# Kernel tuning notes

Hardware: AMD Instinct MI355X
Metric: run time of the kernel (lower is better)

Reference implementation:

```python
import jax, jax.numpy as jnp
import numpy as np

BLOCK_LEN = 64

def _segsum(x):
    # x: (..., T) -> (..., T, T) with entry [t, s] = sum_{u=s+1..t} x[u], -inf above diagonal
    T = x.shape[-1]
    cs = jnp.cumsum(x, axis=-1)
    ss = cs[..., :, None] - cs[..., None, :]
    mask = jnp.tril(jnp.ones((T, T), dtype=bool))
    return jnp.where(mask, ss, -jnp.inf)

def setup_inputs() -> dict:
    key = jax.random.key(0)
    kx, ka, kb, kc = jax.random.split(key, 4)
    b, L, h, p, n = 4, 4096, 32, 64, 16
    X = jax.random.normal(kx, (b, L, h, p), dtype=jnp.float32)
    # negative, small-magnitude A so exp(cumsum(A)) stays finite (decaying SSM),
    # matching the math of the module while keeping the baseline numerically sane
    A = -0.1 * jnp.abs(jax.random.normal(ka, (b, L, h), dtype=jnp.float32))
    B = jax.random.normal(kb, (b, L, h, n), dtype=jnp.float32)
    C = jax.random.normal(kc, (b, L, h, n), dtype=jnp.float32)
    return {"X": X, "A": A, "B": B, "C": C}

def reference(X, A, B, C):
    b, L, h, p = X.shape
    n = B.shape[-1]
    l = BLOCK_LEN
    c = L // l
    # chunk into blocks
    Xb = X.reshape(b, c, l, h, p)                       # b c l h p
    Ab = A.reshape(b, c, l, h).transpose(0, 3, 1, 2)    # b h c l
    Bb = B.reshape(b, c, l, h, n)                       # b c l h n
    Cb = C.reshape(b, c, l, h, n)                       # b c l h n
    A_cumsum = jnp.cumsum(Ab, axis=-1)                  # b h c l
    # intra-chunk (diagonal) term; equals the fused per-timestep scan
    # h_t = exp(A_t)*h_{t-1} + B_t*x_t ; y_t = C_t . h_t
    Lmat = jnp.exp(_segsum(Ab))                         # b h c l l (lower-tri)
    Y_diag = jnp.einsum('bclhn,bcshn,bhcls,bcshp->bclhp', Cb, Bb, Lmat, Xb)
    # per-chunk end states
    decay_states = jnp.exp(A_cumsum[..., -1:] - A_cumsum)  # b h c l
    states = jnp.einsum('bclhn,bhcl,bclhp->bchpn', Bb, decay_states, Xb)
    states = jnp.concatenate([jnp.zeros_like(states[:, :1]), states], axis=1)  # b (c+1) h p n
    # inter-chunk recurrence via segment-sum of chunk totals
    decay_chunk = jnp.exp(_segsum(jnp.pad(A_cumsum[..., -1], ((0, 0), (0, 0), (1, 0)))))  # b h (c+1) (c+1)
    new_states = jnp.einsum('bhzc,bchpn->bzhpn', decay_chunk, states)
    states = new_states[:, :-1]                          # b c h p n
    # state -> output contribution
    state_decay_out = jnp.exp(A_cumsum)                  # b h c l
    Y_off = jnp.einsum('bclhn,bchpn,bhcl->bclhp', Cb, states, state_decay_out)
    return (Y_diag + Y_off).reshape(b, L, h, p)
```

## Files before the change

### kernel.cpp

```cpp
#include <hip/hip_runtime.h>

#define BATCH   4
#define SEQLEN  4096
#define NHEADS  32
#define PDIM    64
#define NDIM    16
#define CHUNK   64
#define NCHUNK  64
#define PHALF   32

typedef short v8s __attribute__((ext_vector_type(8)));
typedef float v4f __attribute__((ext_vector_type(4)));

union V8U { v8s s; unsigned u[4]; };

__device__ __forceinline__ short f2bf(float f) {
    union { float f; unsigned u; } x; x.f = f;
    unsigned r = (x.u + 0x7FFFu + ((x.u >> 16) & 1u)) >> 16;
    return (short)r;
}
__device__ __forceinline__ float bf2f(short s) {
    union { unsigned u; float f; } x; x.u = ((unsigned)(unsigned short)s) << 16;
    return x.f;
}
__device__ __forceinline__ unsigned cvt_pk_bf16(float lo, float hi) {
    unsigned r;
    asm("v_cvt_pk_bf16_f32 %0, %1, %2" : "=v"(r) : "v"(lo), "v"(hi));
    return r;
}

__device__ __forceinline__ float wave_iscan(float v, int lane) {
#pragma unroll
    for (int d = 1; d < 64; d <<= 1) {
        float o = __shfl_up(v, (unsigned)d, 64);
        if (lane >= d) v += o;
    }
    return v;
}

__global__ __launch_bounds__(512) void k_fused(
    const float* __restrict__ X, const float* __restrict__ A,
    const float* __restrict__ Bm, const float* __restrict__ Cm,
    float* __restrict__ Y)
{
    const int ph = blockIdx.x, hh = blockIdx.y, bb = blockIdx.z;
    const int tid = threadIdx.x;
    const int lane = tid & 63;
    const int wv = tid >> 6;
    const int W = wv & 3;
    const int qq = lane >> 4, nn = lane & 15;

    __shared__ __align__(16) float sCumAll[SEQLEN];
    __shared__ __align__(16) short xF [4][4][64][8];
    __shared__ __align__(16) short xSF[4][4][64][8];
    __shared__ __align__(16) short cFq[4][2048];
    __shared__ __align__(16) short bFq[4][2048];
    __shared__ __align__(16) short bFs[4][1024];
    __shared__ __align__(16) short sF [4][1024];
    __shared__ __align__(16) float gRaw[CHUNK][68];
    __shared__ float wtot[8];

    {
        const v8s z8 = {0,0,0,0,0,0,0,0};
        ((v8s*)cFq)[tid] = z8; ((v8s*)cFq)[tid + 512] = z8;
        ((v8s*)bFq)[tid] = z8; ((v8s*)bFq)[tid + 512] = z8;
        if (tid < 128) ((v8s*)sF)[tid] = z8;
    }

    {
        const float* Ab = A + (size_t)bb * SEQLEN * NHEADS + hh;
        const int tb = wv * 512 + lane * 8;
        float av[8];
#pragma unroll
        for (int j = 0; j < 8; ++j) av[j] = Ab[(size_t)(tb + j) * NHEADS];
        float s8 = 0.f;
#pragma unroll
        for (int j = 0; j < 8; ++j) s8 += av[j];
        const float pre = wave_iscan(s8, lane);
        if (lane == 63) wtot[wv] = pre;
        __syncthreads();
        float base = 0.f;
#pragma unroll
        for (int w = 0; w < 7; ++w) if (w < wv) base += wtot[w];
        float c = base + pre - s8;
#pragma unroll
        for (int j = 0; j < 8; ++j) { c += av[j]; sCumAll[tb + j] = c; }
        __syncthreads();
    }

    auto stage = [&](int c, int buf) {
        const int t0c = bb * SEQLEN + c * CHUNK;
        const float* gcc = &sCumAll[c * CHUNK];
        const int ti = wv - 4, kk = ti >> 1, nt = ti & 1;
        const int trow = kk * 32 + qq * 8;
        const float* xb = X + ((size_t)(t0c + trow) * NHEADS + hh) * PDIM
                            + ph * PHALF + nt * 16 + nn;
        float xv[8];
#pragma unroll
        for (int j = 0; j < 8; ++j) xv[j] = xb[(size_t)j * (NHEADS * PDIM)];
        const float gtot = gcc[63];
        float ex[8];
#pragma unroll
        for (int j = 0; j < 8; ++j) ex[j] = __expf(gtot - gcc[trow + j]);
        V8U xf, xs;
#pragma unroll
        for (int j2 = 0; j2 < 4; ++j2) {
            xf.u[j2] = cvt_pk_bf16(xv[2*j2], xv[2*j2+1]);
            xs.u[j2] = cvt_pk_bf16(xv[2*j2] * ex[2*j2], xv[2*j2+1] * ex[2*j2+1]);
        }
        *(v8s*)&xF [buf][kk*2+nt][lane][0] = xf.s;
        *(v8s*)&xSF[buf][kk*2+nt][lane][0] = xs.s;
        const int ptid = tid & 255;
        const int r = ptid >> 2, n0 = (ptid & 3) * 4;
        const float4 bv = *(const float4*)&Bm[((size_t)(t0c + r) * NHEADS + hh) * NDIM + n0];
        const int offq = ((r >> 4) * 64 + (n0 >> 3) * 16 + (r & 15)) * 8 + (n0 & 7);
        bFq[buf][offq + 0] = f2bf(bv.x); bFq[buf][offq + 1] = f2bf(bv.y);
        bFq[buf][offq + 2] = f2bf(bv.z); bFq[buf][offq + 3] = f2bf(bv.w);
        const int kb = r >> 5, qb = (r >> 3) & 3, jj = r & 7;
        const int bs = (kb * 64 + qb * 16) * 8 + jj;
        bFs[buf][bs + (n0 + 0) * 8] = f2bf(bv.x);
        bFs[buf][bs + (n0 + 1) * 8] = f2bf(bv.y);
        bFs[buf][bs + (n0 + 2) * 8] = f2bf(bv.z);
        bFs[buf][bs + (n0 + 3) * 8] = f2bf(bv.w);
        const float4 cv = *(const float4*)&Cm[((size_t)(t0c + r) * NHEADS + hh) * NDIM + n0];
        cFq[buf][offq + 0] = f2bf(cv.x); cFq[buf][offq + 1] = f2bf(cv.y);
        cFq[buf][offq + 2] = f2bf(cv.z); cFq[buf][offq + 3] = f2bf(cv.w);
    };

    const v4f zero = {0.f, 0.f, 0.f, 0.f};

    auto qk_g = [&](const float* gc, int buf) -> v8s {
        const v8s cfrag = *(const v8s*)&cFq[buf][(W * 64 + lane) * 8];
        float tc[4];
#pragma unroll
        for (int r = 0; r < 4; ++r) tc[r] = gc[W * 16 + qq * 4 + r];
#pragma unroll
        for (int st = 0; st < 4; ++st) {
            if (st <= W) {
                const v8s bfrag = *(const v8s*)&bFq[buf][(st * 64 + lane) * 8];
                v4f acc = __builtin_amdgcn_mfma_f32_16x16x32_bf16(cfrag, bfrag, zero, 0, 0, 0);
                const float cums = gc[st * 16 + nn];
#pragma unroll
                for (int r = 0; r < 4; ++r) {
                    const int t = W * 16 + qq * 4 + r;
                    const int s = st * 16 + nn;
                    gRaw[t][s] = (t >= s) ? acc[r] * __expf(tc[r] - cums) : 0.f;
                }
            }
        }
        if (W == 0) {
#pragma unroll
            for (int r = 0; r < 4; ++r) gRaw[qq * 4 + r][16 + nn] = 0.f;
        } else if (W == 2) {
#pragma unroll
            for (int r = 0; r < 4; ++r) gRaw[32 + qq * 4 + r][48 + nn] = 0.f;
        }
        return cfrag;
    };

    auto do_y = [&](const float* gc, float gbase, int buf, int t0c, v8s cfrag) {
        const float et = __expf(gc[W * 16 + nn] - gbase);
        V8U cef;
#pragma unroll
        for (int j2 = 0; j2 < 4; ++j2)
            cef.u[j2] = cvt_pk_bf16(bf2f(cfrag[2*j2]) * et, bf2f(cfrag[2*j2+1]) * et);
        V8U ga0u, ga1u;
        {
            const float* gr = &gRaw[W * 16 + nn][qq * 8];
#pragma unroll
            for (int j2 = 0; j2 < 4; ++j2) ga0u.u[j2] = cvt_pk_bf16(gr[2*j2], gr[2*j2+1]);
        }
        const bool usekk1 = (W >= 2);
        if (usekk1) {
            const float* gr = &gRaw[W * 16 + nn][32 + qq * 8];
#pragma unroll
            for (int j2 = 0; j2 < 4; ++j2) ga1u.u[j2] = cvt_pk_bf16(gr[2*j2], gr[2*j2+1]);
        }
        v4f ya[2];
#pragma unroll
        for (int nt2 = 0; nt2 < 2; ++nt2) {
            const v8s sfrag = *(const v8s*)&sF[buf][(nt2 * 64 + lane) * 8];
            v4f a = __builtin_amdgcn_mfma_f32_16x16x32_bf16(cef.s, sfrag, zero, 0, 0, 0);
            const v8s x0 = *(const v8s*)&xF[buf][0 + nt2][lane][0];
            a = __builtin_amdgcn_mfma_f32_16x16x32_bf16(ga0u.s, x0, a, 0, 0, 0);
            if (usekk1) {
                const v8s x1 = *(const v8s*)&xF[buf][2 + nt2][lane][0];
                a = __builtin_amdgcn_mfma_f32_16x16x32_bf16(ga1u.s, x1, a, 0, 0, 0);
            }
            ya[nt2] = a;
        }
#pragma unroll
        for (int r = 0; r < 4; ++r) {
            const int t = W * 16 + qq * 4 + r;
            float* yp = Y + ((size_t)(t0c + t) * NHEADS + hh) * PDIM + ph * PHALF + nn;
            yp[0]  = ya[0][r];
            yp[16] = ya[1][r];
        }
    };

    if (wv >= 4) { stage(0, 0); stage(1, 1); }
    __syncthreads();

    v4f S = {0.f, 0.f, 0.f, 0.f};

#pragma unroll 1
    for (int k = 0; k < NCHUNK; ++k) {
        const int buf = k & 3;
        const float* gc = &sCumAll[k * CHUNK];
        const float gbase = (k == 0) ? 0.f : gc[-1];

        if (wv >= 4) {
            if (k + 2 < NCHUNK) stage(k + 2, (k + 2) & 3);
            if (wv < 6) {
                const int Wp = wv - 4;
                const v8s a0 = *(const v8s*)&xSF[buf][0 + Wp][lane][0];
                const v8s a1 = *(const v8s*)&xSF[buf][2 + Wp][lane][0];
                const v8s b0 = *(const v8s*)&bFs[buf][(0 * 64 + lane) * 8];
                const v8s b1 = *(const v8s*)&bFs[buf][(1 * 64 + lane) * 8];
                v4f sa = __builtin_amdgcn_mfma_f32_16x16x32_bf16(a0, b0, zero, 0, 0, 0);
                sa = __builtin_amdgcn_mfma_f32_16x16x32_bf16(a1, b1, sa, 0, 0, 0);
                const float Et = __expf(gc[63] - gbase);
#pragma unroll
                for (int r = 0; r < 4; ++r) S[r] = Et * S[r] + sa[r];
                short* d = &sF[(k + 1) & 3][0];
#pragma unroll
                for (int r = 0; r < 4; ++r)
                    d[(Wp * 64 + (nn >> 3) * 16 + qq * 4 + r) * 8 + (nn & 7)] = f2bf(S[r]);
            }
        } else {
            __builtin_amdgcn_s_setprio(1);
            const int t0c = bb * SEQLEN + k * CHUNK;
            const v8s cfrag = qk_g(gc, buf);
            do_y(gc, gbase, buf, t0c, cfrag);
            __builtin_amdgcn_s_setprio(0);
        }
        __syncthreads();
    }
}

extern "C" void kernel_launch(void* const* d_in, const int* in_sizes, int n_in,
                              void* d_out, int out_size, void* d_ws, size_t ws_size,
                              hipStream_t stream) {
    const float* X  = (const float*)d_in[0];
    const float* A  = (const float*)d_in[1];
    const float* Bm = (const float*)d_in[2];
    const float* Cm = (const float*)d_in[3];
    float* Y = (float*)d_out;
    (void)d_ws; (void)ws_size;

    dim3 grid(2, NHEADS, BATCH);
    k_fused<<<grid, 512, 0, stream>>>(X, A, Bm, Cm, Y);
}
```

Baseline: 313.7 us.

## Prefetch next chunk into registers, pack bf16 stores, factor exponentials

Splits the producer staging into a global-load phase and an LDS-write phase so the loads for chunk k+3 are in flight while chunk k is computed. This hides global memory latency from the producer waves. The B/C conversions now use packed bf16 conversions with 64-bit LDS stores. The per-element exp(tc-cums) in the intra-chunk decay is factored into per-row and per-column exponentials relative to gbase. The loop-end __syncthreads is replaced with an explicit lgkmcnt wait plus s_barrier, which avoids waiting on outstanding global loads. In exchange it costs extra registers, and the factored exponentials could overflow or lose precision.

```diff
diff --git a/kernel.cpp b/kernel.cpp
--- a/kernel.cpp
+++ b/kernel.cpp
@@ -88,16 +88,27 @@
         __syncthreads();
     }
 
-    auto stage = [&](int c, int buf) {
+    float pxv[8];
+    float4 pbv, pcv;
+
+    auto loadc = [&](int c) {
         const int t0c = bb * SEQLEN + c * CHUNK;
-        const float* gcc = &sCumAll[c * CHUNK];
         const int ti = wv - 4, kk = ti >> 1, nt = ti & 1;
         const int trow = kk * 32 + qq * 8;
         const float* xb = X + ((size_t)(t0c + trow) * NHEADS + hh) * PDIM
                             + ph * PHALF + nt * 16 + nn;
-        float xv[8];
-#pragma unroll
-        for (int j = 0; j < 8; ++j) xv[j] = xb[(size_t)j * (NHEADS * PDIM)];
+#pragma unroll
+        for (int j = 0; j < 8; ++j) pxv[j] = xb[(size_t)j * (NHEADS * PDIM)];
+        const int ptid = tid & 255;
+        const int r = ptid >> 2, n0 = (ptid & 3) * 4;
+        pbv = *(const float4*)&Bm[((size_t)(t0c + r) * NHEADS + hh) * NDIM + n0];
+        pcv = *(const float4*)&Cm[((size_t)(t0c + r) * NHEADS + hh) * NDIM + n0];
+    };
+
+    auto writec = [&](int c, int buf) {
+        const float* gcc = &sCumAll[c * CHUNK];
+        const int ti = wv - 4, kk = ti >> 1, nt = ti & 1;
+        const int trow = kk * 32 + qq * 8;
         const float gtot = gcc[63];
         float ex[8];
 #pragma unroll
@@ -105,46 +116,46 @@
         V8U xf, xs;
 #pragma unroll
         for (int j2 = 0; j2 < 4; ++j2) {
-            xf.u[j2] = cvt_pk_bf16(xv[2*j2], xv[2*j2+1]);
-            xs.u[j2] = cvt_pk_bf16(xv[2*j2] * ex[2*j2], xv[2*j2+1] * ex[2*j2+1]);
+            xf.u[j2] = cvt_pk_bf16(pxv[2*j2], pxv[2*j2+1]);
+            xs.u[j2] = cvt_pk_bf16(pxv[2*j2] * ex[2*j2], pxv[2*j2+1] * ex[2*j2+1]);
         }
         *(v8s*)&xF [buf][kk*2+nt][lane][0] = xf.s;
         *(v8s*)&xSF[buf][kk*2+nt][lane][0] = xs.s;
         const int ptid = tid & 255;
         const int r = ptid >> 2, n0 = (ptid & 3) * 4;
-        const float4 bv = *(const float4*)&Bm[((size_t)(t0c + r) * NHEADS + hh) * NDIM + n0];
         const int offq = ((r >> 4) * 64 + (n0 >> 3) * 16 + (r & 15)) * 8 + (n0 & 7);
-        bFq[buf][offq + 0] = f2bf(bv.x); bFq[buf][offq + 1] = f2bf(bv.y);
-        bFq[buf][offq + 2] = f2bf(bv.z); bFq[buf][offq + 3] = f2bf(bv.w);
+        const unsigned b01 = cvt_pk_bf16(pbv.x, pbv.y), b23 = cvt_pk_bf16(pbv.z, pbv.w);
+        const unsigned c01 = cvt_pk_bf16(pcv.x, pcv.y), c23 = cvt_pk_bf16(pcv.z, pcv.w);
+        uint2 bq; bq.x = b01; bq.y = b23;
+        uint2 cq; cq.x = c01; cq.y = c23;
+        *(uint2*)&bFq[buf][offq] = bq;
+        *(uint2*)&cFq[buf][offq] = cq;
         const int kb = r >> 5, qb = (r >> 3) & 3, jj = r & 7;
         const int bs = (kb * 64 + qb * 16) * 8 + jj;
-        bFs[buf][bs + (n0 + 0) * 8] = f2bf(bv.x);
-        bFs[buf][bs + (n0 + 1) * 8] = f2bf(bv.y);
-        bFs[buf][bs + (n0 + 2) * 8] = f2bf(bv.z);
-        bFs[buf][bs + (n0 + 3) * 8] = f2bf(bv.w);
-        const float4 cv = *(const float4*)&Cm[((size_t)(t0c + r) * NHEADS + hh) * NDIM + n0];
-        cFq[buf][offq + 0] = f2bf(cv.x); cFq[buf][offq + 1] = f2bf(cv.y);
-        cFq[buf][offq + 2] = f2bf(cv.z); cFq[buf][offq + 3] = f2bf(cv.w);
+        bFs[buf][bs + (n0 + 0) * 8] = (short)(b01 & 0xFFFF);
+        bFs[buf][bs + (n0 + 1) * 8] = (short)(b01 >> 16);
+        bFs[buf][bs + (n0 + 2) * 8] = (short)(b23 & 0xFFFF);
+        bFs[buf][bs + (n0 + 3) * 8] = (short)(b23 >> 16);
     };
 
     const v4f zero = {0.f, 0.f, 0.f, 0.f};
 
-    auto qk_g = [&](const float* gc, int buf) -> v8s {
+    auto qk_g = [&](const float* gc, float gbase, int buf) -> v8s {
         const v8s cfrag = *(const v8s*)&cFq[buf][(W * 64 + lane) * 8];
-        float tc[4];
-#pragma unroll
-        for (int r = 0; r < 4; ++r) tc[r] = gc[W * 16 + qq * 4 + r];
+        float er[4];
+#pragma unroll
+        for (int r = 0; r < 4; ++r) er[r] = __expf(gc[W * 16 + qq * 4 + r] - gbase);
 #pragma unroll
         for (int st = 0; st < 4; ++st) {
             if (st <= W) {
                 const v8s bfrag = *(const v8s*)&bFq[buf][(st * 64 + lane) * 8];
                 v4f acc = __builtin_amdgcn_mfma_f32_16x16x32_bf16(cfrag, bfrag, zero, 0, 0, 0);
-                const float cums = gc[st * 16 + nn];
+                const float ec = __expf(gbase - gc[st * 16 + nn]);
 #pragma unroll
                 for (int r = 0; r < 4; ++r) {
                     const int t = W * 16 + qq * 4 + r;
                     const int s = st * 16 + nn;
-                    gRaw[t][s] = (t >= s) ? acc[r] * __expf(tc[r] - cums) : 0.f;
+                    gRaw[t][s] = (t >= s) ? acc[r] * er[r] * ec : 0.f;
                 }
             }
         }
@@ -198,7 +209,11 @@
         }
     };
 
-    if (wv >= 4) { stage(0, 0); stage(1, 1); }
+    if (wv >= 4) {
+        loadc(0); writec(0, 0);
+        loadc(1); writec(1, 1);
+        loadc(2);
+    }
     __syncthreads();
 
     v4f S = {0.f, 0.f, 0.f, 0.f};
@@ -210,7 +225,8 @@
         const float gbase = (k == 0) ? 0.f : gc[-1];
 
         if (wv >= 4) {
-            if (k + 2 < NCHUNK) stage(k + 2, (k + 2) & 3);
+            if (k + 2 < NCHUNK) writec(k + 2, (k + 2) & 3);
+            if (k + 3 < NCHUNK) loadc(k + 3);
             if (wv < 6) {
                 const int Wp = wv - 4;
                 const v8s a0 = *(const v8s*)&xSF[buf][0 + Wp][lane][0];
@@ -230,11 +246,14 @@
         } else {
             __builtin_amdgcn_s_setprio(1);
             const int t0c = bb * SEQLEN + k * CHUNK;
-            const v8s cfrag = qk_g(gc, buf);
+            const v8s cfrag = qk_g(gc, gbase, buf);
             do_y(gc, gbase, buf, t0c, cfrag);
             __builtin_amdgcn_s_setprio(0);
         }
-        __syncthreads();
+
+        asm volatile("s_waitcnt lgkmcnt(0)" ::: "memory");
+        __builtin_amdgcn_s_barrier();
+        asm volatile("" ::: "memory");
     }
 }
 
```

Result: faster. 299.9 us (-4.4%).
